# Kernel optimization log

Measured on AMD Instinct MI355X. Metric: run time of the kernel, lower is better.

The kernel has to match this reference:

```python
import jax, jax.numpy as jnp
import numpy as np

B, C, H, W = 4, 256, 64, 64
R = 8          # rank = min(8, C//4)
G = 4          # conv groups
CG = C // G    # channels per group


def conv1x1(x, w, b):
    # x: [B,C,H,W], w: [O,C], b: [O]
    return jnp.einsum('oc,bchw->bohw', w, x) + b[None, :, None, None]


def conv1x1_grouped(x, w, b):
    # x: [B,C,H,W], w: [C, C//G] (per-output-channel slice of its group), b: [C]
    xg = x.reshape(B, G, CG, H, W)
    wg = w.reshape(G, CG, CG)  # [group, out_in_group, in_in_group]
    out = jnp.einsum('goc,bgchw->bgohw', wg, xg).reshape(B, C, H, W)
    return out + b[None, :, None, None]


def attend(q, k, v):
    # q,k: [B,R,H,W]; v: [B,C,H,W]; N = H*W
    qf = q.reshape(B, R, H * W)
    kf = k.reshape(B, R, H * W)
    vf = v.reshape(B, C, H * W)
    scores = jnp.einsum('bri,brj->bij', qf, kf)       # [B,N,N], no 1/sqrt scaling (faithful)
    attn = jax.nn.softmax(scores, axis=-1)
    out = jnp.einsum('bcm,bmn->bcn', vf, attn)        # v @ attn, contraction over query index m
    return out.reshape(B, C, H, W)


def setup_inputs():
    key = jax.random.key(0)
    ks = jax.random.split(key, 10)
    s = 0.05
    return {
        'fL': jax.random.normal(ks[0], (B, C, H, W), jnp.float32),
        'fU': jax.random.normal(ks[1], (B, C, H, W), jnp.float32),
        'qL_w': jax.random.normal(ks[2], (R, C), jnp.float32) * s,
        'qL_b': jnp.zeros((R,), jnp.float32),
        'kU_w': jax.random.normal(ks[3], (R, C), jnp.float32) * s,
        'kU_b': jnp.zeros((R,), jnp.float32),
        'vU_w': jax.random.normal(ks[4], (C, CG), jnp.float32) * s,
        'vU_b': jnp.zeros((C,), jnp.float32),
        'qU_w': jax.random.normal(ks[5], (R, C), jnp.float32) * s,
        'qU_b': jnp.zeros((R,), jnp.float32),
        'kL_w': jax.random.normal(ks[6], (R, C), jnp.float32) * s,
        'kL_b': jnp.zeros((R,), jnp.float32),
        'vL_w': jax.random.normal(ks[7], (C, CG), jnp.float32) * s,
        'vL_b': jnp.zeros((C,), jnp.float32),
        'beta': jnp.array(0.5, jnp.float32),
    }


def reference(fL, fU, qL_w, qL_b, kU_w, kU_b, vU_w, vU_b,
              qU_w, qU_b, kL_w, kL_b, vL_w, vL_b, beta):
    LU = attend(conv1x1(fL, qL_w, qL_b),
                conv1x1(fU, kU_w, kU_b),
                conv1x1_grouped(fU, vU_w, vU_b))
    UL = attend(conv1x1(fU, qU_w, qU_b),
                conv1x1(fL, kL_w, kL_b),
                conv1x1_grouped(fL, vL_w, vL_b))
    fL2 = fL + beta * LU
    fU2 = fU + beta * UL
    return (fL2, fU2)
```

## Files before the change

kernel.cpp:

```cpp
#include <hip/hip_runtime.h>

typedef float f32x4 __attribute__((ext_vector_type(4)));
typedef float f32x16 __attribute__((ext_vector_type(16)));
typedef short s16x8 __attribute__((ext_vector_type(8)));
typedef unsigned short u16;
typedef unsigned long long u64;

#define BN 4
#define CC 256
#define NN 4096

static __device__ __forceinline__ u16 f2bf(float x) {
    unsigned int u = __float_as_uint(x);
    u += 0x7FFF + ((u >> 16) & 1);
    return (u16)(u >> 16);
}

__global__ __launch_bounds__(256) void k_wtrans(
    const float* __restrict__ qLw, const float* __restrict__ kLw,
    const float* __restrict__ qUw, const float* __restrict__ kUw,
    const float* __restrict__ vUw, const float* __restrict__ vLw,
    float* __restrict__ wT, float* __restrict__ wvT)
{
    int a = blockIdx.x, t = threadIdx.x;
    const float* qw = a ? qUw : qLw;
    const float* kw = a ? kUw : kLw;
#pragma unroll
    for (int r = 0; r < 8; ++r) {
        wT[((size_t)a * 256 + t) * 16 + r]     = qw[r * 256 + t];
        wT[((size_t)a * 256 + t) * 16 + 8 + r] = kw[r * 256 + t];
    }
    const float* wv = a ? vLw : vUw;
    for (int cp = 0; cp < 64; ++cp)
        wvT[((size_t)a * 64 + cp) * 256 + t] = wv[(size_t)t * 64 + cp];
}

__global__ __launch_bounds__(512) void k_qkprep(
    const float* __restrict__ fL, const float* __restrict__ fU,
    const float* __restrict__ wT,
    const float* __restrict__ qLb, const float* __restrict__ kLb,
    const float* __restrict__ qUb, const float* __restrict__ kUb,
    u16* __restrict__ qbf, u16* __restrict__ kbf)
{
    int blk = blockIdx.x;
    int nc = blk & 31, b = (blk >> 5) & 3, src = blk >> 7;
    const float* f = src ? fU : fL;
    int qa = src, ka = 1 - src;
    int t = threadIdx.x;
    int nl = t & 127;
    int cs = __builtin_amdgcn_readfirstlane(t >> 7) * 64;
    int n = nc * 128 + nl;
    const float* fp = f + (size_t)b * 256 * NN + n;
    const float* wbase = wT + (size_t)src * 4096;

    float acc[16];
#pragma unroll
    for (int r = 0; r < 16; ++r) acc[r] = 0.f;

#pragma unroll 4
    for (int c = cs; c < cs + 64; ++c) {
        float fv = fp[(size_t)c * NN];
        const float* wr = wbase + (size_t)c * 16;
#pragma unroll
        for (int r = 0; r < 16; ++r) acc[r] += wr[r] * fv;
    }

    __shared__ float red[4][128][17];
    int cc = t >> 7;
#pragma unroll
    for (int r = 0; r < 16; ++r) red[cc][nl][r] = acc[r];
    __syncthreads();

    if (t < 128) {
        const float* bq = src ? qUb : qLb;
        const float* bk = src ? kUb : kLb;
        const float L2E = 1.4426950408889634f;
        int nn = nc * 128 + t;
        u16 pq[8], pk[8];
#pragma unroll
        for (int r = 0; r < 8; ++r) {
            float sq = red[0][t][r] + red[1][t][r] + red[2][t][r] + red[3][t][r];
            float sk = red[0][t][8+r] + red[1][t][8+r] + red[2][t][8+r] + red[3][t][8+r];
            pq[r] = f2bf((sq + bq[r]) * L2E);
            pk[r] = f2bf( sk + bk[r]);
        }
        uint4 vq, vk;
        vq.x = pq[0] | ((unsigned)pq[1] << 16); vq.y = pq[2] | ((unsigned)pq[3] << 16);
        vq.z = pq[4] | ((unsigned)pq[5] << 16); vq.w = pq[6] | ((unsigned)pq[7] << 16);
        vk.x = pk[0] | ((unsigned)pk[1] << 16); vk.y = pk[2] | ((unsigned)pk[3] << 16);
        vk.z = pk[4] | ((unsigned)pk[5] << 16); vk.w = pk[6] | ((unsigned)pk[7] << 16);
        *(uint4*)(qbf + (((size_t)qa * BN + b) * NN + nn) * 8) = vq;
        *(uint4*)(kbf + (((size_t)ka * BN + b) * NN + nn) * 8) = vk;
    }
}

__global__ __launch_bounds__(256) void k_zsum(
    const u16* __restrict__ qbf, const u16* __restrict__ kbf,
    float* __restrict__ Z)
{
    int blk = blockIdx.x;
    int mt = blk & 31, ab = blk >> 5;
    int t = threadIdx.x, l = t & 63;
    int w = __builtin_amdgcn_readfirstlane(t >> 6);
    int l31 = l & 31, g2 = l >> 5;
    int m0 = mt * 128 + w * 32;

    const u16* qab = qbf + (size_t)ab * NN * 8;
    const u16* kab = kbf + (size_t)ab * NN * 8;

    s16x8 af = *(const s16x8*)(qab + (size_t)(m0 + l31) * 8);
    if (g2) af = (s16x8)0;

    auto ldb = [&](int i) -> s16x8 {
        s16x8 r = *(const s16x8*)(kab + (size_t)(i * 32 + l31) * 8);
        return g2 ? (s16x8)0 : r;
    };

    float zp[16];
#pragma unroll
    for (int r = 0; r < 16; ++r) zp[r] = 0.f;

    s16x8 b0 = ldb(0), b1 = ldb(1);
#pragma unroll 1
    for (int i = 0; i < 128; ++i) {
        int nx = i + 2 < 127 ? i + 2 : 127;
        s16x8 bn = ldb(nx);
        f32x16 s = __builtin_amdgcn_mfma_f32_32x32x16_bf16(af, b0, (f32x16)0.f, 0, 0, 0);
#pragma unroll
        for (int r = 0; r < 16; ++r) zp[r] += __builtin_exp2f(s[r]);
        b0 = b1; b1 = bn;
    }

#pragma unroll
    for (int r = 0; r < 16; ++r) {
        float v = zp[r];
#pragma unroll
        for (int d = 1; d < 32; d <<= 1) v += __shfl_xor(v, d, 64);
        zp[r] = v;
    }
    if (l31 == 0) {
#pragma unroll
        for (int r = 0; r < 16; ++r) {
            int m = m0 + (r & 3) + 8 * (r >> 2) + 4 * g2;
            Z[(size_t)ab * NN + m] = zp[r];
        }
    }
}

__global__ __launch_bounds__(256) void k_vprep(
    const float* __restrict__ fL, const float* __restrict__ fU,
    const float* __restrict__ wvT,
    const float* __restrict__ vUb, const float* __restrict__ vLb,
    const float* __restrict__ Z, u16* __restrict__ vpt)
{
    int blk = blockIdx.x;
    int mc = blk & 31, g = (blk >> 5) & 3, ab = blk >> 7;
    int a = ab >> 2, b = ab & 3;
    const float* f    = a ? fL : fU;
    const float* bias = a ? vLb : vUb;
    int t = threadIdx.x, l = t & 63;
    int wu = __builtin_amdgcn_readfirstlane(t >> 6);
    int m0 = mc * 128 + l * 2;

    const float* fg = f + ((size_t)b * 256 + g * 64) * NN + m0;
    const float* wq = wvT + (size_t)a * 16384 + g * 64 + wu * 16;

    float acc[16][2];
#pragma unroll
    for (int j = 0; j < 16; ++j) { acc[j][0] = 0.f; acc[j][1] = 0.f; }

    for (int cp = 0; cp < 64; ++cp) {
        float2 fv = *(const float2*)(fg + (size_t)cp * NN);
        const float* wr = wq + (size_t)cp * 256;
        float4 w0 = *(const float4*)(wr);
        float4 w1 = *(const float4*)(wr + 4);
        float4 w2 = *(const float4*)(wr + 8);
        float4 w3 = *(const float4*)(wr + 12);
        float wv[16] = {w0.x,w0.y,w0.z,w0.w, w1.x,w1.y,w1.z,w1.w,
                        w2.x,w2.y,w2.z,w2.w, w3.x,w3.y,w3.z,w3.w};
#pragma unroll
        for (int j = 0; j < 16; ++j) {
            acc[j][0] += wv[j] * fv.x;
            acc[j][1] += wv[j] * fv.y;
        }
    }

    float2 z = *(const float2*)(Z + (size_t)ab * NN + m0);
    float zr0 = 1.f / z.x, zr1 = 1.f / z.y;
    int mt = m0 >> 5, mi = m0 & 31;
    u16* vpo = vpt + (((size_t)ab * 128 + mt) * 256 + g * 64 + wu * 16) * 32 + mi;
#pragma unroll
    for (int j = 0; j < 16; ++j) {
        float bj = bias[g * 64 + wu * 16 + j];
        unsigned pk = (unsigned)f2bf((acc[j][0] + bj) * zr0) |
                      ((unsigned)f2bf((acc[j][1] + bj) * zr1) << 16);
        *(unsigned*)(vpo + (size_t)j * 32) = pk;
    }
}

__global__ __launch_bounds__(512) void k_main(
    const float* __restrict__ fL, const float* __restrict__ fU,
    const u16* __restrict__ qbf, const u16* __restrict__ kbf,
    const u16* __restrict__ vpt, const float* __restrict__ beta_p,
    float* __restrict__ out)
{
    int blk = blockIdx.x;
    int ab = blk & 7, nt = blk >> 3;
    int a = ab >> 2, b = ab & 3;
    int n0 = nt * 128;
    int t = threadIdx.x, l = t & 63;
    int w = __builtin_amdgcn_readfirstlane(t >> 6);
    int c15 = l & 15, g = l >> 4;
    int swz = (c15 & 7) << 4;

    __shared__ u16 ebuf[2][128][64];

    auto eptr = [&](int p, int n, int mbyte) -> char* {
        return ((char*)ebuf) + (((p << 7) + n) << 7) + (mbyte ^ swz);
    };

    const u16* qab = qbf + (size_t)ab * NN * 8;
    const u16* kab = kbf + (size_t)ab * NN * 8;

    s16x8 bkf = *(const s16x8*)(kab + (size_t)(n0 + w * 16 + c15) * 8);
    if (g) bkf = (s16x8)0;

    const u16* apb = vpt + (size_t)ab * (128ull * 8192)
                   + (size_t)(w * 32 + c15) * 32 + g * 8;

    f32x4 acc[2][8];
#pragma unroll
    for (int i = 0; i < 2; ++i)
#pragma unroll
        for (int j = 0; j < 8; ++j) acc[i][j] = (f32x4)0.f;

    auto qld = [&](int win, int mq) -> s16x8 {
        s16x8 r = *(const s16x8*)(qab + (size_t)(win * 64 + mq * 16 + c15) * 8);
        return g ? (s16x8)0 : r;
    };

    auto egen = [&](int pbuf, const s16x8 (&qv)[4]) {
#pragma unroll
        for (int mq = 0; mq < 4; ++mq) {
            f32x4 s = __builtin_amdgcn_mfma_f32_16x16x32_bf16(qv[mq], bkf, (f32x4)0.f, 0, 0, 0);
            float e0 = __builtin_exp2f(s[0]);
            float e1 = __builtin_exp2f(s[1]);
            float e2 = __builtin_exp2f(s[2]);
            float e3 = __builtin_exp2f(s[3]);
            unsigned lo, hi;
            asm("v_cvt_pk_bf16_f32 %0, %1, %2" : "=v"(lo) : "v"(e0), "v"(e1));
            asm("v_cvt_pk_bf16_f32 %0, %1, %2" : "=v"(hi) : "v"(e2), "v"(e3));
            uint2 pk; pk.x = lo; pk.y = hi;
            *(uint2*)eptr(pbuf, w * 16 + c15, mq * 32 + g * 8) = pk;
        }
    };

    s16x8 qn[4];
    s16x8 afc[2][2], afn[2][2];

    auto step = [&](int P, int kn, int kq, bool do_egen) {
        const u16* apn = apb + (size_t)(2 * kn) * 8192;
#pragma unroll
        for (int cf = 0; cf < 2; ++cf) {
            afn[cf][0] = *(const s16x8*)(apn + cf * 512);
            afn[cf][1] = *(const s16x8*)(apn + 8192 + cf * 512);
        }
        s16x8 bf[8];
#pragma unroll
        for (int nf = 0; nf < 8; ++nf)
            bf[nf] = *(const s16x8*)eptr(P, nf * 16 + c15, g * 16);
        if (do_egen) egen(P ^ 1, qn);
#pragma unroll
        for (int cf = 0; cf < 2; ++cf)
#pragma unroll
            for (int nf = 0; nf < 8; ++nf)
                acc[cf][nf] = __builtin_amdgcn_mfma_f32_16x16x32_bf16(
                    afc[cf][0], bf[nf], acc[cf][nf], 0, 0, 0);
#pragma unroll
        for (int nf = 0; nf < 8; ++nf)
            bf[nf] = *(const s16x8*)eptr(P, nf * 16 + c15, 64 + g * 16);
#pragma unroll
        for (int cf = 0; cf < 2; ++cf)
#pragma unroll
            for (int nf = 0; nf < 8; ++nf)
                acc[cf][nf] = __builtin_amdgcn_mfma_f32_16x16x32_bf16(
                    afc[cf][1], bf[nf], acc[cf][nf], 0, 0, 0);
#pragma unroll
        for (int mq = 0; mq < 4; ++mq) qn[mq] = qld(kq, mq);
#pragma unroll
        for (int cf = 0; cf < 2; ++cf) {
            afc[cf][0] = afn[cf][0];
            afc[cf][1] = afn[cf][1];
        }
        __syncthreads();
    };

    {
        s16x8 q0[4];
#pragma unroll
        for (int mq = 0; mq < 4; ++mq) q0[mq] = qld(0, mq);
        egen(0, q0);
    }
#pragma unroll
    for (int mq = 0; mq < 4; ++mq) qn[mq] = qld(1, mq);
#pragma unroll
    for (int cf = 0; cf < 2; ++cf) {
        afc[cf][0] = *(const s16x8*)(apb + cf * 512);
        afc[cf][1] = *(const s16x8*)(apb + 8192 + cf * 512);
    }
    __syncthreads();

#pragma unroll 1
    for (int k2 = 0; k2 < 32; ++k2) {
        int ke = 2 * k2;
        step(0, ke + 1, ke + 2 < 63 ? ke + 2 : 63, true);
        int ko = 2 * k2 + 1;
        int kn = ko + 1 < 63 ? ko + 1 : 63;
        step(1, kn, ko + 2 < 63 ? ko + 2 : 63, k2 < 31);
    }

    float beta = beta_p[0];
    const float* base = a ? fU : fL;
    float* op = out + (size_t)a * ((size_t)BN * CC * NN);
#pragma unroll
    for (int cf = 0; cf < 2; ++cf)
#pragma unroll
        for (int nf = 0; nf < 8; ++nf)
#pragma unroll
            for (int r = 0; r < 4; ++r) {
                int c = w * 32 + cf * 16 + g * 4 + r;
                int n = n0 + nf * 16 + c15;
                size_t idx = ((size_t)b * CC + c) * NN + n;
                op[idx] = base[idx] + beta * acc[cf][nf][r];
            }
}

extern "C" void kernel_launch(void* const* d_in, const int* in_sizes, int n_in,
                              void* d_out, int out_size, void* d_ws, size_t ws_size,
                              hipStream_t stream) {
    const float* fL  = (const float*)d_in[0];
    const float* fU  = (const float*)d_in[1];
    const float* qLw = (const float*)d_in[2];
    const float* qLb = (const float*)d_in[3];
    const float* kUw = (const float*)d_in[4];
    const float* kUb = (const float*)d_in[5];
    const float* vUw = (const float*)d_in[6];
    const float* vUb = (const float*)d_in[7];
    const float* qUw = (const float*)d_in[8];
    const float* qUb = (const float*)d_in[9];
    const float* kLw = (const float*)d_in[10];
    const float* kLb = (const float*)d_in[11];
    const float* vLw = (const float*)d_in[12];
    const float* vLb = (const float*)d_in[13];
    const float* beta = (const float*)d_in[14];

    char* ws = (char*)d_ws;
    float* wT  = (float*)(ws);
    float* wvT = (float*)(ws + 32768);
    u16*   qbf = (u16*)  (ws + 163840);
    u16*   kbf = (u16*)  (ws + 688128);
    float* Z   = (float*)(ws + 1212416);
    u16*   vpt = (u16*)  (ws + 1343488);
    float* out = (float*)d_out;

    k_wtrans<<<2, 256, 0, stream>>>(qLw, kLw, qUw, kUw, vUw, vLw, wT, wvT);
    k_qkprep<<<256, 512, 0, stream>>>(fL, fU, wT, qLb, kLb, qUb, kUb, qbf, kbf);
    k_zsum<<<256, 256, 0, stream>>>(qbf, kbf, Z);
    k_vprep<<<1024, 256, 0, stream>>>(fL, fU, wvT, vUb, vLb, Z, vpt);
    k_main<<<256, 512, 0, stream>>>(fL, fU, qbf, kbf, vpt, beta, out);
}
```

Measured before the change: 180.3 us.

## Halve k_main output tile to 64 columns, double grid, and ping-pong register buffers

k_main now computes 64 output columns per block instead of 128 and launches 512 blocks instead of 256. This gives more blocks than the 256 CUs and asks for 4 blocks per CU through launch bounds. The exp-generation work is split so 4 wave groups each cover 16 columns and 2 halves of the m-window, which halves the per-wave egen load. Register ping-pong buffers replace the copy of the next A fragments, and s_setprio is raised around MFMA bursts. In exchange, the A (vpt) fragment reads from global memory double overall, since each block still loads the full channel range for half as many columns.

```diff
diff --git a/kernel.cpp b/kernel.cpp
--- a/kernel.cpp
+++ b/kernel.cpp
@@ -198,7 +198,7 @@
     }
 }
 
-__global__ __launch_bounds__(512) void k_main(
+__global__ __launch_bounds__(512, 4) void k_main(
     const float* __restrict__ fL, const float* __restrict__ fU,
     const u16* __restrict__ qbf, const u16* __restrict__ kbf,
     const u16* __restrict__ vpt, const float* __restrict__ beta_p,
@@ -207,42 +207,45 @@
     int blk = blockIdx.x;
     int ab = blk & 7, nt = blk >> 3;
     int a = ab >> 2, b = ab & 3;
-    int n0 = nt * 128;
+    int n0 = nt * 64;
     int t = threadIdx.x, l = t & 63;
     int w = __builtin_amdgcn_readfirstlane(t >> 6);
     int c15 = l & 15, g = l >> 4;
+    int ng = w & 3;
+    int mh = w >> 2;
     int swz = (c15 & 7) << 4;
 
-    __shared__ u16 ebuf[2][128][64];
+    __shared__ u16 ebuf[2][64][64];
 
     auto eptr = [&](int p, int n, int mbyte) -> char* {
-        return ((char*)ebuf) + (((p << 7) + n) << 7) + (mbyte ^ swz);
+        return ((char*)ebuf) + (p << 13) + (n << 7) + (mbyte ^ swz);
     };
 
     const u16* qab = qbf + (size_t)ab * NN * 8;
     const u16* kab = kbf + (size_t)ab * NN * 8;
 
-    s16x8 bkf = *(const s16x8*)(kab + (size_t)(n0 + w * 16 + c15) * 8);
+    s16x8 bkf = *(const s16x8*)(kab + (size_t)(n0 + ng * 16 + c15) * 8);
     if (g) bkf = (s16x8)0;
 
     const u16* apb = vpt + (size_t)ab * (128ull * 8192)
                    + (size_t)(w * 32 + c15) * 32 + g * 8;
 
-    f32x4 acc[2][8];
+    f32x4 acc[2][4];
 #pragma unroll
     for (int i = 0; i < 2; ++i)
 #pragma unroll
-        for (int j = 0; j < 8; ++j) acc[i][j] = (f32x4)0.f;
-
-    auto qld = [&](int win, int mq) -> s16x8 {
-        s16x8 r = *(const s16x8*)(qab + (size_t)(win * 64 + mq * 16 + c15) * 8);
+        for (int j = 0; j < 4; ++j) acc[i][j] = (f32x4)0.f;
+
+    auto qld = [&](int win, int mq2) -> s16x8 {
+        s16x8 r = *(const s16x8*)(qab + (size_t)(win * 64 + (mh * 2 + mq2) * 16 + c15) * 8);
         return g ? (s16x8)0 : r;
     };
 
-    auto egen = [&](int pbuf, const s16x8 (&qv)[4]) {
-#pragma unroll
-        for (int mq = 0; mq < 4; ++mq) {
-            f32x4 s = __builtin_amdgcn_mfma_f32_16x16x32_bf16(qv[mq], bkf, (f32x4)0.f, 0, 0, 0);
+    auto egen = [&](int pbuf, const s16x8& q0, const s16x8& q1) {
+#pragma unroll
+        for (int mq2 = 0; mq2 < 2; ++mq2) {
+            f32x4 s = __builtin_amdgcn_mfma_f32_16x16x32_bf16(
+                mq2 ? q1 : q0, bkf, (f32x4)0.f, 0, 0, 0);
             float e0 = __builtin_exp2f(s[0]);
             float e1 = __builtin_exp2f(s[1]);
             float e2 = __builtin_exp2f(s[2]);
@@ -251,72 +254,69 @@
             asm("v_cvt_pk_bf16_f32 %0, %1, %2" : "=v"(lo) : "v"(e0), "v"(e1));
             asm("v_cvt_pk_bf16_f32 %0, %1, %2" : "=v"(hi) : "v"(e2), "v"(e3));
             uint2 pk; pk.x = lo; pk.y = hi;
-            *(uint2*)eptr(pbuf, w * 16 + c15, mq * 32 + g * 8) = pk;
-        }
-    };
-
-    s16x8 qn[4];
-    s16x8 afc[2][2], afn[2][2];
-
-    auto step = [&](int P, int kn, int kq, bool do_egen) {
+            *(uint2*)eptr(pbuf, ng * 16 + c15, (mh * 2 + mq2) * 32 + g * 8) = pk;
+        }
+    };
+
+    auto step = [&](int P, int kwin,
+                    s16x8 (&aC)[2][2], s16x8 (&aN)[2][2],
+                    s16x8 (&qC)[2], s16x8 (&qN)[2], bool doeg) {
+        int kn = kwin + 1 < 63 ? kwin + 1 : 63;
         const u16* apn = apb + (size_t)(2 * kn) * 8192;
 #pragma unroll
         for (int cf = 0; cf < 2; ++cf) {
-            afn[cf][0] = *(const s16x8*)(apn + cf * 512);
-            afn[cf][1] = *(const s16x8*)(apn + 8192 + cf * 512);
-        }
-        s16x8 bf[8];
-#pragma unroll
-        for (int nf = 0; nf < 8; ++nf)
+            aN[cf][0] = *(const s16x8*)(apn + cf * 512);
+            aN[cf][1] = *(const s16x8*)(apn + 8192 + cf * 512);
+        }
+        int kq = kwin + 2 < 63 ? kwin + 2 : 63;
+        qN[0] = qld(kq, 0);
+        qN[1] = qld(kq, 1);
+
+        s16x8 bf[4];
+#pragma unroll
+        for (int nf = 0; nf < 4; ++nf)
             bf[nf] = *(const s16x8*)eptr(P, nf * 16 + c15, g * 16);
-        if (do_egen) egen(P ^ 1, qn);
+        if (doeg) egen(P ^ 1, qC[0], qC[1]);
+        __builtin_amdgcn_s_setprio(1);
 #pragma unroll
         for (int cf = 0; cf < 2; ++cf)
 #pragma unroll
-            for (int nf = 0; nf < 8; ++nf)
+            for (int nf = 0; nf < 4; ++nf)
                 acc[cf][nf] = __builtin_amdgcn_mfma_f32_16x16x32_bf16(
-                    afc[cf][0], bf[nf], acc[cf][nf], 0, 0, 0);
-#pragma unroll
-        for (int nf = 0; nf < 8; ++nf)
+                    aC[cf][0], bf[nf], acc[cf][nf], 0, 0, 0);
+        __builtin_amdgcn_s_setprio(0);
+#pragma unroll
+        for (int nf = 0; nf < 4; ++nf)
             bf[nf] = *(const s16x8*)eptr(P, nf * 16 + c15, 64 + g * 16);
+        __builtin_amdgcn_s_setprio(1);
 #pragma unroll
         for (int cf = 0; cf < 2; ++cf)
 #pragma unroll
-            for (int nf = 0; nf < 8; ++nf)
+            for (int nf = 0; nf < 4; ++nf)
                 acc[cf][nf] = __builtin_amdgcn_mfma_f32_16x16x32_bf16(
-                    afc[cf][1], bf[nf], acc[cf][nf], 0, 0, 0);
-#pragma unroll
-        for (int mq = 0; mq < 4; ++mq) qn[mq] = qld(kq, mq);
-#pragma unroll
-        for (int cf = 0; cf < 2; ++cf) {
-            afc[cf][0] = afn[cf][0];
-            afc[cf][1] = afn[cf][1];
-        }
+                    aC[cf][1], bf[nf], acc[cf][nf], 0, 0, 0);
+        __builtin_amdgcn_s_setprio(0);
         __syncthreads();
     };
 
     {
-        s16x8 q0[4];
-#pragma unroll
-        for (int mq = 0; mq < 4; ++mq) q0[mq] = qld(0, mq);
-        egen(0, q0);
-    }
-#pragma unroll
-    for (int mq = 0; mq < 4; ++mq) qn[mq] = qld(1, mq);
+        s16x8 z0 = qld(0, 0), z1 = qld(0, 1);
+        egen(0, z0, z1);
+    }
+    s16x8 qA[2], qB[2];
+    qA[0] = qld(1, 0); qA[1] = qld(1, 1);
+    s16x8 afA[2][2], afB[2][2];
 #pragma unroll
     for (int cf = 0; cf < 2; ++cf) {
-        afc[cf][0] = *(const s16x8*)(apb + cf * 512);
-        afc[cf][1] = *(const s16x8*)(apb + 8192 + cf * 512);
+        afA[cf][0] = *(const s16x8*)(apb + cf * 512);
+        afA[cf][1] = *(const s16x8*)(apb + 8192 + cf * 512);
     }
     __syncthreads();
 
 #pragma unroll 1
     for (int k2 = 0; k2 < 32; ++k2) {
-        int ke = 2 * k2;
-        step(0, ke + 1, ke + 2 < 63 ? ke + 2 : 63, true);
-        int ko = 2 * k2 + 1;
-        int kn = ko + 1 < 63 ? ko + 1 : 63;
-        step(1, kn, ko + 2 < 63 ? ko + 2 : 63, k2 < 31);
+        step(0, 2 * k2,     afA, afB, qA, qB, true);
+        step(1, 2 * k2 + 1, afB, afA, qB, qA, k2 < 31);
     }
 
     float beta = beta_p[0];
@@ -325,7 +325,7 @@
 #pragma unroll
     for (int cf = 0; cf < 2; ++cf)
 #pragma unroll
-        for (int nf = 0; nf < 8; ++nf)
+        for (int nf = 0; nf < 4; ++nf)
 #pragma unroll
             for (int r = 0; r < 4; ++r) {
                 int c = w * 32 + cf * 16 + g * 4 + r;
@@ -367,5 +367,5 @@
     k_qkprep<<<256, 512, 0, stream>>>(fL, fU, wT, qLb, kLb, qUb, kUb, qbf, kbf);
     k_zsum<<<256, 256, 0, stream>>>(qbf, kbf, Z);
     k_vprep<<<1024, 256, 0, stream>>>(fL, fU, wvT, vUb, vLb, Z, vpt);
-    k_main<<<256, 512, 0, stream>>>(fL, fU, qbf, kbf, vpt, beta, out);
-}
+    k_main<<<512, 512, 0, stream>>>(fL, fU, qbf, kbf, vpt, beta, out);
+}
```

New measurement: 177.0 us. About the same (-1.8%).
